# Kernel tuning notes

Hardware: AMD Instinct MI355X
Metric: run time of the kernel (lower is better)

The kernel has to match this reference:

```python
import jax, jax.numpy as jnp
import numpy as np

N_NODES = 50000
N_EDGES = 800000
D = 128          # embed_dim
H = 8            # heads
C = D // H       # per-head channels
F = 512          # ff_hidden_dim
LN_EPS = 1e-5
NEG_SLOPE = 0.2  # PyG GATConv default negative_slope


def _layernorm(x, g, b):
    mu = jnp.mean(x, axis=-1, keepdims=True)
    var = jnp.mean(jnp.square(x - mu), axis=-1, keepdims=True)
    return (x - mu) * jax.lax.rsqrt(var + LN_EPS) * g + b


def _gat_conv(x, edge_index, W, att_src, att_dst, bias):
    # PyG GATConv (concat=True, add_self_loops=True, shared lin for src/dst)
    N = x.shape[0]
    xl = (x @ W.T).reshape(N, H, C)                 # [N,H,C]
    a_s = jnp.sum(xl * att_src, axis=-1)            # [N,H]
    a_d = jnp.sum(xl * att_dst, axis=-1)            # [N,H]
    loops = jnp.arange(N)
    src = jnp.concatenate([edge_index[0], loops])   # [E+N]
    dst = jnp.concatenate([edge_index[1], loops])
    e = jax.nn.leaky_relu(a_s[src] + a_d[dst], NEG_SLOPE)  # [E+N,H]
    # segment softmax over incoming edges per destination node
    m = jax.ops.segment_max(e, dst, num_segments=N)
    m = jnp.where(jnp.isfinite(m), m, jnp.zeros_like(m))
    ex = jnp.exp(e - m[dst])
    s = jax.ops.segment_sum(ex, dst, num_segments=N)
    alpha = ex / (s[dst] + 1e-16)                   # [E+N,H]
    msg = xl[src] * alpha[:, :, None]               # [E+N,H,C]
    out = jax.ops.segment_sum(msg, dst, num_segments=N)  # [N,H,C]
    return out.reshape(N, H * C) + bias


def setup_inputs() -> dict:
    key = jax.random.key(0)
    ks = jax.random.split(key, 12)
    sc_d = 1.0 / np.sqrt(D)
    sc_f = 1.0 / np.sqrt(F)
    return {
        "x": jax.random.normal(ks[0], (N_NODES, D), dtype=jnp.float32),
        "virtual_edge_index": jax.random.randint(ks[1], (2, N_EDGES), 0, N_NODES, dtype=jnp.int64),
        "W_gat": jax.random.normal(ks[2], (H * C, D), dtype=jnp.float32) * sc_d,
        "att_src": jax.random.normal(ks[3], (H, C), dtype=jnp.float32) * sc_d,
        "att_dst": jax.random.normal(ks[4], (H, C), dtype=jnp.float32) * sc_d,
        "bias_gat": jnp.zeros((H * C,), dtype=jnp.float32),
        "W1": jax.random.normal(ks[5], (F, D), dtype=jnp.float32) * sc_d,
        "b1": jnp.zeros((F,), dtype=jnp.float32),
        "W2": jax.random.normal(ks[6], (D, F), dtype=jnp.float32) * sc_f,
        "b2": jnp.zeros((D,), dtype=jnp.float32),
        "g1": jnp.ones((D,), dtype=jnp.float32),
        "beta1": jnp.zeros((D,), dtype=jnp.float32),
        "g2": jnp.ones((D,), dtype=jnp.float32),
        "beta2": jnp.zeros((D,), dtype=jnp.float32),
    }


def reference(x, virtual_edge_index, W_gat, att_src, att_dst, bias_gat,
              W1, b1, W2, b2, g1, beta1, g2, beta2):
    h_gat = _gat_conv(x, virtual_edge_index, W_gat, att_src, att_dst, bias_gat)
    h = _layernorm(x + h_gat, g1, beta1)
    h_ff = jax.nn.relu(h @ W1.T + b1) @ W2.T + b2
    return _layernorm(h + h_ff, g2, beta2)
```

## Files before the change

### kernel.cpp

```cpp
#include <hip/hip_runtime.h>
#include <hip/hip_bf16.h>

#define N_NODES 50000
#define N_EDGES 800000
#define N_TOT   850000
#define DIM 128
#define HEADS 8
#define CH 16
#define FF 512
#define LN_EPS 1e-5f
#define NEG_SLOPE 0.2f

#define PART    8
#define NCHUNK  128
#define CHUNK_E (N_EDGES / NCHUNK)
#define NPP     (N_NODES / PART)
#define NHIST   (PART * NCHUNK)

typedef __bf16 bf16x8 __attribute__((ext_vector_type(8)));
typedef float f32x4 __attribute__((ext_vector_type(4)));

__device__ __forceinline__ float bfr2f(unsigned short u) {
  return __uint_as_float(((unsigned)u) << 16);
}
__device__ __forceinline__ unsigned short f2bfr(float f) {
  __hip_bfloat16 h = __float2bfloat16(f);
  return *(unsigned short*)&h;
}
__device__ __forceinline__ float bf2f(__hip_bfloat16 h) { return __bfloat162float(h); }
__device__ __forceinline__ __hip_bfloat16 f2bf(float f) { return __float2bfloat16(f); }

__device__ __forceinline__ bf16x8 ldcvt8(const float* __restrict__ p) {
  const float4 a = ((const float4*)p)[0];
  const float4 b = ((const float4*)p)[1];
  bf16x8 r;
  r[0] = (__bf16)a.x; r[1] = (__bf16)a.y; r[2] = (__bf16)a.z; r[3] = (__bf16)a.w;
  r[4] = (__bf16)b.x; r[5] = (__bf16)b.y; r[6] = (__bf16)b.z; r[7] = (__bf16)b.w;
  return r;
}

__device__ __forceinline__ int ld_src(const int* ei, int mode, int e) {
  int v = mode ? ei[2 * e] : ei[e];
  return min(max(v, 0), N_NODES - 1);
}
__device__ __forceinline__ int ld_dst(const int* ei, int mode, int e) {
  int v = mode ? ei[2 * (N_EDGES + e)] : ei[N_EDGES + e];
  return min(max(v, 0), N_NODES - 1);
}
__device__ __forceinline__ int edge_mode(const int* __restrict__ ei) {
  int any = 0;
  for (int k = 1; k < 64; k += 2) any |= ei[k];
  return (any == 0) ? 1 : 0;
}

__device__ __forceinline__ float expleaky(float v) {
  v = v > 0.f ? v : NEG_SLOPE * v;
  return __expf(v);
}

__global__ __launch_bounds__(256) void k_xl(const float* __restrict__ x,
                                            const float* __restrict__ Wg,
                                            const float* __restrict__ att_s,
                                            const float* __restrict__ att_d,
                                            __hip_bfloat16* __restrict__ xl,
                                            float* __restrict__ a_s,
                                            float* __restrict__ a_d) {
  int gid = blockIdx.x * 256 + threadIdx.x;
  int w = gid >> 6;
  if (w >= 3125 * 2) return;
  int l = threadIdx.x & 63, quad = l >> 4, r = l & 15;
  int strip = w >> 1, cc = w & 1;
  f32x4 acc[4];
#pragma unroll
  for (int t = 0; t < 4; ++t) acc[t] = (f32x4){0.f, 0.f, 0.f, 0.f};
  int arow = strip * 16 + r;
  bf16x8 af[4];
#pragma unroll
  for (int kk = 0; kk < 4; ++kk) af[kk] = ldcvt8(x + arow * DIM + kk * 32 + quad * 8);
#pragma unroll
  for (int kk = 0; kk < 4; ++kk) {
    bf16x8 bfr[4];
#pragma unroll
    for (int t = 0; t < 4; ++t)
      bfr[t] = ldcvt8(Wg + (cc * 64 + t * 16 + r) * DIM + kk * 32 + quad * 8);
#pragma unroll
    for (int t = 0; t < 4; ++t)
      acc[t] = __builtin_amdgcn_mfma_f32_16x16x32_bf16(af[kk], bfr[t], acc[t], 0, 0, 0);
  }
  float ats[4], atd[4];
#pragma unroll
  for (int t = 0; t < 4; ++t) {
    ats[t] = att_s[(cc * 4 + t) * CH + r];
    atd[t] = att_d[(cc * 4 + t) * CH + r];
  }
#pragma unroll
  for (int t = 0; t < 4; ++t)
#pragma unroll
    for (int j = 0; j < 4; ++j) {
      int row = strip * 16 + quad * 4 + j;
      int col = cc * 64 + t * 16 + r;
      xl[row * DIM + col] = f2bf(acc[t][j]);
      float vs = acc[t][j] * ats[t];
      float vd = acc[t][j] * atd[t];
      vs += __shfl_xor(vs, 1); vd += __shfl_xor(vd, 1);
      vs += __shfl_xor(vs, 2); vd += __shfl_xor(vd, 2);
      vs += __shfl_xor(vs, 4); vd += __shfl_xor(vd, 4);
      vs += __shfl_xor(vs, 8); vd += __shfl_xor(vd, 8);
      if (r == 0) {
        a_s[row * 8 + cc * 4 + t] = vs;
        a_d[row * 8 + cc * 4 + t] = vd;
      }
    }
}

__global__ __launch_bounds__(256) void k_hist2(const int* __restrict__ ei,
                                               const float* __restrict__ W1,
                                               const float* __restrict__ W2,
                                               __hip_bfloat16* __restrict__ wb,
                                               unsigned short* __restrict__ blkh) {
  __shared__ unsigned int hist[NPP];
  int p = blockIdx.x & 7, c = blockIdx.x >> 3;
  int tid = threadIdx.x;
  int gi = blockIdx.x * 256 + tid;
  if (gi < 65536)        wb[gi] = f2bf(W1[gi]);
  else if (gi < 131072)  wb[gi] = f2bf(W2[gi - 65536]);
  for (int i = tid; i < NPP; i += 256) hist[i] = 0;
  int m = edge_mode(ei);
  __syncthreads();
  int nlo = p * NPP;
  int e1 = (c + 1) * CHUNK_E;
  for (int e = c * CHUNK_E + tid; e < e1; e += 256) {
    int d = ld_dst(ei, m, e) - nlo;
    if ((unsigned)d < (unsigned)NPP) atomicAdd(&hist[d], 1u);
  }
  __syncthreads();
  unsigned short* dst = blkh + (size_t)c * N_NODES + nlo;
  for (int i = tid; i < NPP; i += 256) dst[i] = (unsigned short)hist[i];
}

__global__ __launch_bounds__(256) void k_nscan(unsigned short* __restrict__ blkh,
                                               int* __restrict__ deg) {
  int n = blockIdx.x * 256 + threadIdx.x;
  if (n >= N_NODES) return;
  int run = 0;
#pragma unroll 8
  for (int c = 0; c < NCHUNK; ++c) {
    unsigned short* ptr = blkh + (size_t)c * N_NODES + n;
    int v = *ptr;
    *ptr = (unsigned short)run;
    run += v;
  }
  deg[n] = run;
}

__global__ __launch_bounds__(1024) void k_scan(const int* __restrict__ deg,
                                               int* __restrict__ offs,
                                               int* __restrict__ eid) {
  __shared__ int wtot[16];
  __shared__ int wbase[16];
  __shared__ int running_s;
  int tid = threadIdx.x, wv = tid >> 6, ln = tid & 63;
  if (tid == 0) running_s = 0;
  __syncthreads();
  for (int base = 0; base < N_NODES; base += 4096) {
    int i0 = base + tid * 4;
    int v0 = 0, v1 = 0, v2 = 0, v3 = 0;
    if (i0 + 3 < N_NODES) {
      int4 dv = *(const int4*)(deg + i0);
      v0 = dv.x + 1; v1 = dv.y + 1; v2 = dv.z + 1; v3 = dv.w + 1;
    } else {
      if (i0 + 0 < N_NODES) v0 = deg[i0 + 0] + 1;
      if (i0 + 1 < N_NODES) v1 = deg[i0 + 1] + 1;
      if (i0 + 2 < N_NODES) v2 = deg[i0 + 2] + 1;
      if (i0 + 3 < N_NODES) v3 = deg[i0 + 3] + 1;
    }
    int tt = v0 + v1 + v2 + v3;
    int xsc = tt;
#pragma unroll
    for (int off = 1; off < 64; off <<= 1) {
      int t = __shfl_up(xsc, off);
      if (ln >= off) xsc += t;
    }
    if (ln == 63) wtot[wv] = xsc;
    __syncthreads();
    if (wv == 0) {
      int t = (ln < 16) ? wtot[ln] : 0;
#pragma unroll
      for (int off = 1; off < 16; off <<= 1) {
        int u = __shfl_up(t, off);
        if (ln >= off) t += u;
      }
      if (ln < 16) wbase[ln] = t;
    }
    __syncthreads();
    int run0 = running_s;
    int excl = run0 + ((wv == 0) ? 0 : wbase[wv - 1]) + xsc - tt;
    if (i0 + 0 < N_NODES) { offs[i0 + 0] = excl; eid[excl] = i0 + 0; }
    excl += v0;
    if (i0 + 1 < N_NODES) { offs[i0 + 1] = excl; eid[excl] = i0 + 1; }
    excl += v1;
    if (i0 + 2 < N_NODES) { offs[i0 + 2] = excl; eid[excl] = i0 + 2; }
    excl += v2;
    if (i0 + 3 < N_NODES) { offs[i0 + 3] = excl; eid[excl] = i0 + 3; }
    __syncthreads();
    if (tid == 1023) running_s = run0 + wbase[15];
  }
  __syncthreads();
  if (tid == 0) offs[N_NODES] = running_s;
}

__global__ __launch_bounds__(256) void k_scatter(const int* __restrict__ ei,
                                                 const int* __restrict__ offs,
                                                 const unsigned short* __restrict__ blkh,
                                                 int* __restrict__ eid) {
  __shared__ unsigned int fill[NPP];
  int p = blockIdx.x & 7, c = blockIdx.x >> 3;
  int tid = threadIdx.x;
  for (int i = tid; i < NPP; i += 256) fill[i] = 0;
  int m = edge_mode(ei);
  __syncthreads();
  int nlo = p * NPP;
  const unsigned short* exl = blkh + (size_t)c * N_NODES;
  int e1 = (c + 1) * CHUNK_E;
  for (int e = c * CHUNK_E + tid; e < e1; e += 256) {
    int dg = ld_dst(ei, m, e);
    int d = dg - nlo;
    if ((unsigned)d < (unsigned)NPP) {
      unsigned ord = atomicAdd(&fill[d], 1u);
      int slot = offs[dg] + 1 + (int)exl[dg] + (int)ord;
      eid[slot] = ld_src(ei, m, e);
    }
  }
}

__global__ __launch_bounds__(256) void k_attn(const int* __restrict__ eid, const int* __restrict__ offs,
                                              const float* __restrict__ a_s,
                                              const float* __restrict__ a_d,
                                              const __hip_bfloat16* __restrict__ xl,
                                              const float* __restrict__ x,
                                              const float* __restrict__ bias,
                                              const float* __restrict__ g1,
                                              const float* __restrict__ be1,
                                              __hip_bfloat16* __restrict__ h1out) {
  int wv = threadIdx.x >> 6, l = threadIdx.x & 63;
  int n = blockIdx.x * 4 + wv;
  int start = offs[n], end = offs[n + 1];
  int h8 = l & 7, sl8 = l >> 3;
  int hq = l >> 3;
  float adv = a_d[n * 8 + h8];

  const char* xlb = (const char*)xl;
  int l4 = 4 * l;
  float sme = 0.f;
  float A0 = 0.f, A1 = 0.f;
  int p = start;
  for (; p + 8 <= end; p += 8) {
    int s = eid[p + sl8];
    int boff = s << 8;
    float w = expleaky(a_s[s * 8 + h8] + adv);
    sme += w;
#pragma unroll
    for (int q = 0; q < 8; ++q) {
      int bq = __shfl(boff, q * 8);
      float wq = __shfl(w, q * 8 + hq);
      ushort2 u = *(const ushort2*)(xlb + bq + l4);
      A0 += wq * bfr2f(u.x);
      A1 += wq * bfr2f(u.y);
    }
  }
  int rem = end - p;
  if (rem > 0) {
    int sl = (sl8 < rem) ? sl8 : 0;
    int s = eid[p + sl];
    int boff = s << 8;
    float w = (sl8 < rem) ? expleaky(a_s[s * 8 + h8] + adv) : 0.f;
    sme += w;
    for (int q = 0; q < rem; ++q) {
      int bq = __shfl(boff, q * 8);
      float wq = __shfl(w, q * 8 + hq);
      ushort2 u = *(const ushort2*)(xlb + bq + l4);
      A0 += wq * bfr2f(u.x);
      A1 += wq * bfr2f(u.y);
    }
  }
  sme += __shfl_xor(sme, 8);
  sme += __shfl_xor(sme, 16);
  sme += __shfl_xor(sme, 32);
  float smh = __shfl(sme, hq);
  float inv = 1.f / (smh + 1e-16f);
  float acc0 = A0 * inv;
  float acc1 = A1 * inv;

  float2 xv = *(const float2*)(x + n * DIM + 2 * l);
  float2 bv = *(const float2*)(bias + 2 * l);
  float v0 = acc0 + bv.x + xv.x;
  float v1 = acc1 + bv.y + xv.y;
  float s2 = v0 + v1;
  for (int off = 32; off >= 1; off >>= 1) s2 += __shfl_xor(s2, off);
  float mu = s2 * (1.f / 128.f);
  float d0 = v0 - mu, d1 = v1 - mu;
  float q = d0 * d0 + d1 * d1;
  for (int off = 32; off >= 1; off >>= 1) q += __shfl_xor(q, off);
  float rs = rsqrtf(q * (1.f / 128.f) + LN_EPS);
  float2 gv = *(const float2*)(g1 + 2 * l);
  float2 bev = *(const float2*)(be1 + 2 * l);
  ushort2 o;
  o.x = f2bfr(d0 * rs * gv.x + bev.x);
  o.y = f2bfr(d1 * rs * gv.y + bev.y);
  *(ushort2*)((unsigned short*)h1out + n * DIM + 2 * l) = o;
}

__global__ __launch_bounds__(256) void k_ffn1(const __hip_bfloat16* __restrict__ h1,
                                              const __hip_bfloat16* __restrict__ W1b,
                                              const float* __restrict__ b1,
                                              __hip_bfloat16* __restrict__ hid,
                                              int row_base) {
  int wv = threadIdx.x >> 6, l = threadIdx.x & 63, quad = l >> 4, r = l & 15;
  int blk = blockIdx.x;
  int base = row_base + blk * 32;
  const __bf16* h1b = (const __bf16*)h1;
  const __bf16* w1 = (const __bf16*)W1b;
  int r0 = min(base + r, N_NODES - 1);
  int r1 = min(base + 16 + r, N_NODES - 1);

  bf16x8 bn[2][4];
#pragma unroll
  for (int kk = 0; kk < 4; ++kk) {
    bn[0][kk] = *(const bf16x8*)(h1b + r0 * DIM + kk * 32 + quad * 8);
    bn[1][kk] = *(const bf16x8*)(h1b + r1 * DIM + kk * 32 + quad * 8);
  }
  f32x4 acc1[8][2];
#pragma unroll
  for (int tm = 0; tm < 8; ++tm)
#pragma unroll
    for (int tn = 0; tn < 2; ++tn) acc1[tm][tn] = (f32x4){0.f, 0.f, 0.f, 0.f};
#pragma unroll
  for (int kk = 0; kk < 4; ++kk) {
    bf16x8 wf[8];
#pragma unroll
    for (int tm = 0; tm < 8; ++tm)
      wf[tm] = *(const bf16x8*)(w1 + (wv * 128 + tm * 16 + r) * DIM + kk * 32 + quad * 8);
#pragma unroll
    for (int tm = 0; tm < 8; ++tm) {
      acc1[tm][0] = __builtin_amdgcn_mfma_f32_16x16x32_bf16(wf[tm], bn[0][kk], acc1[tm][0], 0, 0, 0);
      acc1[tm][1] = __builtin_amdgcn_mfma_f32_16x16x32_bf16(wf[tm], bn[1][kk], acc1[tm][1], 0, 0, 0);
    }
  }
  unsigned short* hb = (unsigned short*)hid;
#pragma unroll
  for (int tm = 0; tm < 8; ++tm) {
    int f0 = wv * 128 + tm * 16 + quad * 4;
    float4 bb = *(const float4*)(b1 + f0);
#pragma unroll
    for (int tn = 0; tn < 2; ++tn) {
      ushort4 o;
      o.x = f2bfr(fmaxf(acc1[tm][tn][0] + bb.x, 0.f));
      o.y = f2bfr(fmaxf(acc1[tm][tn][1] + bb.y, 0.f));
      o.z = f2bfr(fmaxf(acc1[tm][tn][2] + bb.z, 0.f));
      o.w = f2bfr(fmaxf(acc1[tm][tn][3] + bb.w, 0.f));
      int idx = ((blk * 2 + tn) * 64 + wv * 16 + tm * 2 + (quad >> 1)) * 128
                + r * 8 + (quad & 1) * 4;
      *(ushort4*)(hb + idx) = o;
    }
  }
}

__global__ __launch_bounds__(256) void k_ffn2(const __hip_bfloat16* __restrict__ hid,
                                              const __hip_bfloat16* __restrict__ W2b,
                                              const float* __restrict__ b2,
                                              const float* __restrict__ g2,
                                              const float* __restrict__ be2,
                                              const __hip_bfloat16* __restrict__ h1,
                                              float* __restrict__ out,
                                              int row_base) {
  __shared__ float ps[4][2][16], pq[4][2][16];
  int wv = threadIdx.x >> 6, l = threadIdx.x & 63, quad = l >> 4, r = l & 15;
  int blk = blockIdx.x;
  int base = row_base + blk * 32;
  const __bf16* w2 = (const __bf16*)W2b;
  const unsigned short* hb = (const unsigned short*)hid;

  f32x4 acc2[2][2];
#pragma unroll
  for (int s = 0; s < 2; ++s)
#pragma unroll
    for (int tn = 0; tn < 2; ++tn) acc2[s][tn] = (f32x4){0.f, 0.f, 0.f, 0.f};

  const unsigned short* a0base = hb + ((blk * 2 + 0) * 64 + quad) * 128 + r * 8;
  const unsigned short* a1base = hb + ((blk * 2 + 1) * 64 + quad) * 128 + r * 8;
  const __bf16* w2base = w2 + (wv * 32 + r) * FF + quad * 8;

#pragma unroll 4
  for (int ka = 0; ka < 16; ++ka) {
    bf16x8 a0 = *(const bf16x8*)(a0base + ka * 512);
    bf16x8 a1 = *(const bf16x8*)(a1base + ka * 512);
    bf16x8 wa0 = *(const bf16x8*)(w2base + ka * 32);
    bf16x8 wa1 = *(const bf16x8*)(w2base + 16 * FF + ka * 32);
    acc2[0][0] = __builtin_amdgcn_mfma_f32_16x16x32_bf16(a0, wa0, acc2[0][0], 0, 0, 0);
    acc2[0][1] = __builtin_amdgcn_mfma_f32_16x16x32_bf16(a0, wa1, acc2[0][1], 0, 0, 0);
    acc2[1][0] = __builtin_amdgcn_mfma_f32_16x16x32_bf16(a1, wa0, acc2[1][0], 0, 0, 0);
    acc2[1][1] = __builtin_amdgcn_mfma_f32_16x16x32_bf16(a1, wa1, acc2[1][1], 0, 0, 0);
  }
#pragma unroll
  for (int s = 0; s < 2; ++s)
#pragma unroll
    for (int tn = 0; tn < 2; ++tn) {
      int col = wv * 32 + tn * 16 + r;
      float b2c = b2[col];
#pragma unroll
      for (int j = 0; j < 4; ++j) {
        int row = min(base + s * 16 + quad * 4 + j, N_NODES - 1);
        acc2[s][tn][j] += b2c + bf2f(h1[row * DIM + col]);
      }
    }
#pragma unroll
  for (int s = 0; s < 2; ++s)
#pragma unroll
    for (int j = 0; j < 4; ++j) {
      float sm = acc2[s][0][j] + acc2[s][1][j];
      float qm = acc2[s][0][j] * acc2[s][0][j] + acc2[s][1][j] * acc2[s][1][j];
      sm += __shfl_xor(sm, 1); sm += __shfl_xor(sm, 2); sm += __shfl_xor(sm, 4); sm += __shfl_xor(sm, 8);
      qm += __shfl_xor(qm, 1); qm += __shfl_xor(qm, 2); qm += __shfl_xor(qm, 4); qm += __shfl_xor(qm, 8);
      if (r == j) { ps[wv][s][quad * 4 + j] = sm; pq[wv][s][quad * 4 + j] = qm; }
    }
  __syncthreads();
#pragma unroll
  for (int s = 0; s < 2; ++s)
#pragma unroll
    for (int j = 0; j < 4; ++j) {
      int row16 = quad * 4 + j;
      float st = (ps[0][s][row16] + ps[1][s][row16]) + (ps[2][s][row16] + ps[3][s][row16]);
      float qt = (pq[0][s][row16] + pq[1][s][row16]) + (pq[2][s][row16] + pq[3][s][row16]);
      float mu = st * (1.f / 128.f);
      float var = qt * (1.f / 128.f) - mu * mu;
      float rs = rsqrtf(var + LN_EPS);
      int grow = base + s * 16 + row16;
      if (grow < N_NODES) {
#pragma unroll
        for (int tn = 0; tn < 2; ++tn) {
          int col = wv * 32 + tn * 16 + r;
          out[grow * DIM + col] = (acc2[s][tn][j] - mu) * rs * g2[col] + be2[col];
        }
      }
    }
}

#define OFF_H1     0u
#define SZ_H1      (50016u * DIM * 2u)
#define OFF_WB     (OFF_H1 + SZ_H1)
#define SZ_WB      262144u
#define OFF_XL     (OFF_WB + SZ_WB)
#define SZ_XL      (N_NODES * DIM * 2u)
#define OFF_AS     (OFF_XL + SZ_XL)
#define SZ_AS      (N_NODES * HEADS * 4u)
#define OFF_AD     (OFF_AS + SZ_AS)
#define OFF_DEG    (OFF_AD + SZ_AS)
#define SZ_DEG     200192u
#define OFF_OFFS   (OFF_DEG + SZ_DEG)
#define SZ_OFFS    200448u
#define OFF_EID    (OFF_OFFS + SZ_OFFS)
#define SZ_EID     3400192u
#define OFF_BLKH   (OFF_EID + SZ_EID)
#define SZ_BLKH    (NCHUNK * (unsigned)N_NODES * 2u)
#define OFF_HID    OFF_XL
#define SZ_HID_FULL  (50016u * FF * 2u)
#define FFN_CHUNK0_BLOCKS 782
#define FFN_CHUNK1_BLOCKS 781
#define FFN_CHUNK0_ROWS   (FFN_CHUNK0_BLOCKS * 32)

extern "C" void kernel_launch(void* const* d_in, const int* in_sizes, int n_in,
                              void* d_out, int out_size, void* d_ws, size_t ws_size,
                              hipStream_t stream) {
  const float* x     = (const float*)d_in[0];
  const int*   ei    = (const int*)d_in[1];
  const float* Wg    = (const float*)d_in[2];
  const float* att_s = (const float*)d_in[3];
  const float* att_d = (const float*)d_in[4];
  const float* bias  = (const float*)d_in[5];
  const float* W1    = (const float*)d_in[6];
  const float* b1    = (const float*)d_in[7];
  const float* W2    = (const float*)d_in[8];
  const float* b2    = (const float*)d_in[9];
  const float* g1    = (const float*)d_in[10];
  const float* be1   = (const float*)d_in[11];
  const float* g2    = (const float*)d_in[12];
  const float* be2   = (const float*)d_in[13];

  char* ws = (char*)d_ws;
  __hip_bfloat16* h1     = (__hip_bfloat16*)(ws + OFF_H1);
  __hip_bfloat16* wbuf   = (__hip_bfloat16*)(ws + OFF_WB);
  __hip_bfloat16* W1b    = wbuf;
  __hip_bfloat16* W2b    = wbuf + 65536;
  __hip_bfloat16* xl     = (__hip_bfloat16*)(ws + OFF_XL);
  float*          a_s    = (float*)(ws + OFF_AS);
  float*          a_d    = (float*)(ws + OFF_AD);
  int*            deg    = (int*)(ws + OFF_DEG);
  int*            offs   = (int*)(ws + OFF_OFFS);
  int*            eid    = (int*)(ws + OFF_EID);
  unsigned short* blkh   = (unsigned short*)(ws + OFF_BLKH);
  __hip_bfloat16* hid    = (__hip_bfloat16*)(ws + OFF_HID);
  float*          out    = (float*)d_out;

  k_xl     <<<1563,  256, 0, stream>>>(x, Wg, att_s, att_d, xl, a_s, a_d);
  k_hist2  <<<NHIST, 256, 0, stream>>>(ei, W1, W2, wbuf, blkh);
  k_nscan  <<<196,   256, 0, stream>>>(blkh, deg);
  k_scan   <<<1,    1024, 0, stream>>>(deg, offs, eid);
  k_scatter<<<NHIST, 256, 0, stream>>>(ei, offs, blkh, eid);
  k_attn   <<<12500, 256, 0, stream>>>(eid, offs, a_s, a_d, xl, x, bias, g1, be1, h1);
  if (ws_size >= (size_t)OFF_HID + SZ_HID_FULL) {
    k_ffn1 <<<1563, 256, 0, stream>>>(h1, W1b, b1, hid, 0);
    k_ffn2 <<<1563, 256, 0, stream>>>(hid, W2b, b2, g2, be2, h1, out, 0);
  } else {
    k_ffn1 <<<FFN_CHUNK0_BLOCKS, 256, 0, stream>>>(h1, W1b, b1, hid, 0);
    k_ffn2 <<<FFN_CHUNK0_BLOCKS, 256, 0, stream>>>(hid, W2b, b2, g2, be2, h1, out, 0);
    k_ffn1 <<<FFN_CHUNK1_BLOCKS, 256, 0, stream>>>(h1, W1b, b1, hid, FFN_CHUNK0_ROWS);
    k_ffn2 <<<FFN_CHUNK1_BLOCKS, 256, 0, stream>>>(hid, W2b, b2, g2, be2, h1, out, FFN_CHUNK0_ROWS);
  }
}
```

Before: 342.0 us.

## Parallelize chunk scan and node offset scan; prefetch next edge batch in attention

The per-node chunk prefix scan now splits its 128 chunks across 4 thread groups per node and also emits per-tile degree totals. This lets the global offset scan run over 196 blocks, each summing the preceding tile totals, instead of one serial 1024-thread block. The attention loop also software-prefetches the next batch of edge ids and source attention scores to hide gather latency. The cost is an extra workspace buffer and redundant tile-total reductions in every block.

```diff
diff --git a/kernel.cpp b/kernel.cpp
--- a/kernel.cpp
+++ b/kernel.cpp
@@ -16,6 +16,7 @@
 #define CHUNK_E (N_EDGES / NCHUNK)
 #define NPP     (N_NODES / PART)
 #define NHIST   (PART * NCHUNK)
+#define NTILE   196
 
 typedef __bf16 bf16x8 __attribute__((ext_vector_type(8)));
 typedef float f32x4 __attribute__((ext_vector_type(4)));
@@ -138,75 +139,88 @@
   for (int i = tid; i < NPP; i += 256) dst[i] = (unsigned short)hist[i];
 }
 
-__global__ __launch_bounds__(256) void k_nscan(unsigned short* __restrict__ blkh,
-                                               int* __restrict__ deg) {
-  int n = blockIdx.x * 256 + threadIdx.x;
-  if (n >= N_NODES) return;
-  int run = 0;
-#pragma unroll 8
-  for (int c = 0; c < NCHUNK; ++c) {
-    unsigned short* ptr = blkh + (size_t)c * N_NODES + n;
-    int v = *ptr;
-    *ptr = (unsigned short)run;
-    run += v;
-  }
-  deg[n] = run;
-}
-
-__global__ __launch_bounds__(1024) void k_scan(const int* __restrict__ deg,
+__global__ __launch_bounds__(1024) void k_nscan2(unsigned short* __restrict__ blkh,
+                                                 int* __restrict__ deg,
+                                                 int* __restrict__ tsum) {
+  __shared__ int gs[4][256];
+  __shared__ int red[4];
+  int tid = threadIdx.x;
+  int nl = tid & 255, g = tid >> 8;
+  int n = blockIdx.x * 256 + nl;
+  unsigned short vv[32];
+  int gsum = 0;
+  if (n < N_NODES) {
+    const unsigned short* base = blkh + (size_t)(g * 32) * N_NODES + n;
+#pragma unroll
+    for (int i = 0; i < 32; ++i) {
+      vv[i] = base[(size_t)i * N_NODES];
+      gsum += (int)vv[i];
+    }
+  }
+  gs[g][nl] = gsum;
+  __syncthreads();
+  int gexcl = 0;
+#pragma unroll
+  for (int j = 0; j < 4; ++j) if (j < g) gexcl += gs[j][nl];
+  int total = gs[0][nl] + gs[1][nl] + gs[2][nl] + gs[3][nl];
+  if (n < N_NODES) {
+    unsigned short* base = blkh + (size_t)(g * 32) * N_NODES + n;
+    int run = gexcl;
+#pragma unroll
+    for (int i = 0; i < 32; ++i) {
+      int t = (int)vv[i];
+      base[(size_t)i * N_NODES] = (unsigned short)run;
+      run += t;
+    }
+    if (g == 0) deg[n] = total;
+  }
+  if (g == 0) {
+    int val = (n < N_NODES) ? total + 1 : 0;
+    int l = tid & 63, wv = tid >> 6;
+#pragma unroll
+    for (int off = 1; off < 64; off <<= 1) val += __shfl_xor(val, off);
+    if (l == 0) red[wv] = val;
+  }
+  __syncthreads();
+  if (tid == 0) tsum[blockIdx.x] = red[0] + red[1] + red[2] + red[3];
+}
+
+__global__ __launch_bounds__(256) void k_offs2(const int* __restrict__ deg,
+                                               const int* __restrict__ tsum,
                                                int* __restrict__ offs,
                                                int* __restrict__ eid) {
-  __shared__ int wtot[16];
-  __shared__ int wbase[16];
-  __shared__ int running_s;
-  int tid = threadIdx.x, wv = tid >> 6, ln = tid & 63;
-  if (tid == 0) running_s = 0;
-  __syncthreads();
-  for (int base = 0; base < N_NODES; base += 4096) {
-    int i0 = base + tid * 4;
-    int v0 = 0, v1 = 0, v2 = 0, v3 = 0;
-    if (i0 + 3 < N_NODES) {
-      int4 dv = *(const int4*)(deg + i0);
-      v0 = dv.x + 1; v1 = dv.y + 1; v2 = dv.z + 1; v3 = dv.w + 1;
-    } else {
-      if (i0 + 0 < N_NODES) v0 = deg[i0 + 0] + 1;
-      if (i0 + 1 < N_NODES) v1 = deg[i0 + 1] + 1;
-      if (i0 + 2 < N_NODES) v2 = deg[i0 + 2] + 1;
-      if (i0 + 3 < N_NODES) v3 = deg[i0 + 3] + 1;
-    }
-    int tt = v0 + v1 + v2 + v3;
-    int xsc = tt;
-#pragma unroll
-    for (int off = 1; off < 64; off <<= 1) {
-      int t = __shfl_up(xsc, off);
-      if (ln >= off) xsc += t;
-    }
-    if (ln == 63) wtot[wv] = xsc;
-    __syncthreads();
-    if (wv == 0) {
-      int t = (ln < 16) ? wtot[ln] : 0;
-#pragma unroll
-      for (int off = 1; off < 16; off <<= 1) {
-        int u = __shfl_up(t, off);
-        if (ln >= off) t += u;
-      }
-      if (ln < 16) wbase[ln] = t;
-    }
-    __syncthreads();
-    int run0 = running_s;
-    int excl = run0 + ((wv == 0) ? 0 : wbase[wv - 1]) + xsc - tt;
-    if (i0 + 0 < N_NODES) { offs[i0 + 0] = excl; eid[excl] = i0 + 0; }
-    excl += v0;
-    if (i0 + 1 < N_NODES) { offs[i0 + 1] = excl; eid[excl] = i0 + 1; }
-    excl += v1;
-    if (i0 + 2 < N_NODES) { offs[i0 + 2] = excl; eid[excl] = i0 + 2; }
-    excl += v2;
-    if (i0 + 3 < N_NODES) { offs[i0 + 3] = excl; eid[excl] = i0 + 3; }
-    __syncthreads();
-    if (tid == 1023) running_s = run0 + wbase[15];
-  }
-  __syncthreads();
-  if (tid == 0) offs[N_NODES] = running_s;
+  __shared__ int wtot[4];
+  __shared__ int red[4];
+  __shared__ int sbase;
+  int tid = threadIdx.x, l = tid & 63, wv = tid >> 6;
+  int bid = blockIdx.x;
+  int part = (tid < bid) ? tsum[tid] : 0;
+#pragma unroll
+  for (int off = 1; off < 64; off <<= 1) part += __shfl_xor(part, off);
+  if (l == 0) red[wv] = part;
+  __syncthreads();
+  if (tid == 0) sbase = (red[0] + red[1]) + (red[2] + red[3]);
+  __syncthreads();
+  int tbase = sbase;
+  int n = bid * 256 + tid;
+  int v = (n < N_NODES) ? deg[n] + 1 : 0;
+  int xx = v;
+#pragma unroll
+  for (int off = 1; off < 64; off <<= 1) {
+    int t = __shfl_up(xx, off);
+    if (l >= off) xx += t;
+  }
+  if (l == 63) wtot[wv] = xx;
+  __syncthreads();
+  int wbase = 0;
+#pragma unroll
+  for (int j = 0; j < 4; ++j) if (j < wv) wbase += wtot[j];
+  int excl = tbase + wbase + xx - v;
+  if (n < N_NODES) {
+    offs[n] = excl;
+    eid[excl] = n;
+    if (n == N_NODES - 1) offs[N_NODES] = excl + v;
+  }
 }
 
 __global__ __launch_bounds__(256) void k_scatter(const int* __restrict__ ei,
@@ -254,18 +268,27 @@
   float sme = 0.f;
   float A0 = 0.f, A1 = 0.f;
   int p = start;
-  for (; p + 8 <= end; p += 8) {
-    int s = eid[p + sl8];
-    int boff = s << 8;
-    float w = expleaky(a_s[s * 8 + h8] + adv);
-    sme += w;
-#pragma unroll
-    for (int q = 0; q < 8; ++q) {
-      int bq = __shfl(boff, q * 8);
-      float wq = __shfl(w, q * 8 + hq);
-      ushort2 u = *(const ushort2*)(xlb + bq + l4);
-      A0 += wq * bfr2f(u.x);
-      A1 += wq * bfr2f(u.y);
+  int pend = start + ((end - start) & ~7);
+  if (p < pend) {
+    int s_nx = eid[p + sl8];
+    float as_nx = a_s[s_nx * 8 + h8];
+    while (p < pend) {
+      int boff = s_nx << 8;
+      float w = expleaky(as_nx + adv);
+      p += 8;
+      if (p < pend) {
+        s_nx = eid[p + sl8];
+        as_nx = a_s[s_nx * 8 + h8];
+      }
+      sme += w;
+#pragma unroll
+      for (int q = 0; q < 8; ++q) {
+        int bq = __shfl(boff, q * 8);
+        float wq = __shfl(w, q * 8 + hq);
+        ushort2 u = *(const ushort2*)(xlb + bq + l4);
+        A0 += wq * bfr2f(u.x);
+        A1 += wq * bfr2f(u.y);
+      }
     }
   }
   int rem = end - p;
@@ -462,6 +485,7 @@
 #define SZ_EID     3400192u
 #define OFF_BLKH   (OFF_EID + SZ_EID)
 #define SZ_BLKH    (NCHUNK * (unsigned)N_NODES * 2u)
+#define OFF_TSUM   (OFF_BLKH + SZ_BLKH)
 #define OFF_HID    OFF_XL
 #define SZ_HID_FULL  (50016u * FF * 2u)
 #define FFN_CHUNK0_BLOCKS 782
@@ -498,15 +522,16 @@
   int*            offs   = (int*)(ws + OFF_OFFS);
   int*            eid    = (int*)(ws + OFF_EID);
   unsigned short* blkh   = (unsigned short*)(ws + OFF_BLKH);
+  int*            tsum   = (int*)(ws + OFF_TSUM);
   __hip_bfloat16* hid    = (__hip_bfloat16*)(ws + OFF_HID);
   float*          out    = (float*)d_out;
 
   k_xl     <<<1563,  256, 0, stream>>>(x, Wg, att_s, att_d, xl, a_s, a_d);
   k_hist2  <<<NHIST, 256, 0, stream>>>(ei, W1, W2, wbuf, blkh);
-  k_nscan  <<<196,   256, 0, stream>>>(blkh, deg);
-  k_scan   <<<1,    1024, 0, stream>>>(deg, offs, eid);
-  k_scatter<<<NHIST, 256, 0, stream>>>(ei, offs, blkh, eid);
-  k_attn   <<<12500, 256, 0, stream>>>(eid, offs, a_s, a_d, xl, x, bias, g1, be1, h1);
+  k_nscan2 <<<NTILE, 1024, 0, stream>>>(blkh, deg, tsum);
+  k_offs2  <<<NTILE,  256, 0, stream>>>(deg, tsum, offs, eid);
+  k_scatter<<<NHIST,  256, 0, stream>>>(ei, offs, blkh, eid);
+  k_attn   <<<12500,  256, 0, stream>>>(eid, offs, a_s, a_d, xl, x, bias, g1, be1, h1);
   if (ws_size >= (size_t)OFF_HID + SZ_HID_FULL) {
     k_ffn1 <<<1563, 256, 0, stream>>>(h1, W1b, b1, hid, 0);
     k_ffn2 <<<1563, 256, 0, stream>>>(hid, W2b, b2, g2, be2, h1, out, 0);
```

Measured after the change: 305.2 us. 1.12x faster.
